# Performance work log

Measured on AMD Instinct MI355X. Metric: run time of the kernel, lower is better.

## Reference

```python
import jax, jax.numpy as jnp
from jax import lax
import numpy as np

N, CIN, COUT, H, W = 8, 64, 64, 256, 256
KH = KW = 3
AUX, HID = 128, 256


def setup_inputs() -> dict:
    key = jax.random.key(0)
    ks = jax.random.split(key, 12)
    k = float(np.sqrt(1.0 / (CIN * KH * KW)))
    inp = {
        "x": jax.random.normal(ks[0], (N, CIN, H, W), jnp.float32),
        "y": jax.random.normal(ks[1], (N, AUX), jnp.float32),
        "weight": jax.random.uniform(ks[2], (COUT, CIN, KH, KW), jnp.float32, -k, k),
        # modulation MLP: Linear(AUX->HID), PReLU, Linear(HID->COUT*CIN), Sigmoid
        "fc_w1": jax.random.normal(ks[3], (HID, AUX), jnp.float32) * 0.05,
        "fc_b1": jax.random.normal(ks[4], (HID,), jnp.float32) * 0.05,
        "fc_prelu": jnp.asarray(0.25, jnp.float32),
        "fc_w2": jax.random.normal(ks[5], (COUT * CIN, HID), jnp.float32) * 0.05,
        "fc_b2": jax.random.normal(ks[6], (COUT * CIN,), jnp.float32) * 0.05,
        # learned-bias MLP: Linear(AUX->HID), PReLU, Linear(HID->COUT)
        "bias_w1": jax.random.normal(ks[7], (HID, AUX), jnp.float32) * 0.05,
        "bias_b1": jax.random.normal(ks[8], (HID,), jnp.float32) * 0.05,
        "bias_prelu": jnp.asarray(0.25, jnp.float32),
        "bias_w2": jax.random.normal(ks[9], (COUT, HID), jnp.float32) * 0.05,
        "bias_b2": jax.random.normal(ks[10], (COUT,), jnp.float32) * 0.05,
    }
    return inp


def _prelu(h, a):
    return jnp.where(h >= 0, h, a * h)


def reference(x, y, weight, fc_w1, fc_b1, fc_prelu, fc_w2, fc_b2,
              bias_w1, bias_b1, bias_prelu, bias_w2, bias_b2):
    n, cin, h_, w_ = x.shape
    cout = weight.shape[0]
    # modulation factors: (N, COUT*CIN), sigmoid activation
    hm = _prelu(y @ fc_w1.T + fc_b1, fc_prelu)
    mod = jax.nn.sigmoid(hm @ fc_w2.T + fc_b2)
    # per-sample modulated kernels: (N, COUT, CIN, KH, KW)
    w_mod = mod.reshape(n, cout, cin, 1, 1) * weight
    # grouped conv with groups = batch, expressed as vmap over batch
    def conv1(xi, wi):  # xi: (CIN,H,W), wi: (COUT,CIN,KH,KW)
        return lax.conv_general_dilated(
            xi[None], wi, window_strides=(1, 1), padding=[(1, 1), (1, 1)],
            rhs_dilation=(1, 1))[0]
    out = jax.vmap(conv1)(x, w_mod)  # (N, COUT, H, W)
    # learned per-sample bias
    hb = _prelu(y @ bias_w1.T + bias_b1, bias_prelu)
    b = hb @ bias_w2.T + bias_b2  # (N, COUT)
    return out + b[:, :, None, None]
```

## Files before the change

kernel.cpp:

```cpp
#include <hip/hip_runtime.h>
#include <hip/hip_bf16.h>


typedef short bf16x8 __attribute__((ext_vector_type(8)));
typedef float f32x16 __attribute__((ext_vector_type(16)));

#define NB 8
#define CIN 64
#define COUT 64
#define HH 256
#define WW 256
#define HWP (HH * WW)
#define AUXD 128
#define HIDD 256

#define XRW8 (258 * 16)
#define XBUF8 (6 * XRW8)
#define WOFF (2 * XBUF8)
#define WUNITS (9 * 8 * 64)
#define SMEMB (WOFF + (WUNITS + 1) * 16)

__device__ __forceinline__ unsigned short f2bf(float f) {
    unsigned u = __builtin_bit_cast(unsigned, f);
    u += 0x7FFFu + ((u >> 16) & 1u);
    return (unsigned short)(u >> 16);
}

__device__ __forceinline__ unsigned pk2(float a, float b, float vm) {
    return (unsigned)f2bf(a * vm) | ((unsigned)f2bf(b * vm) << 16);
}

__global__ __launch_bounds__(256) void mlp_kernel(
    const float* __restrict__ y, const float* __restrict__ weight,
    const float* __restrict__ fc_w1, const float* __restrict__ fc_b1,
    const float* __restrict__ fc_prelu,
    const float* __restrict__ fc_w2, const float* __restrict__ fc_b2,
    const float* __restrict__ bias_w1, const float* __restrict__ bias_b1,
    const float* __restrict__ bias_prelu,
    const float* __restrict__ bias_w2, const float* __restrict__ bias_b2,
    unsigned short* __restrict__ w_bf, float* __restrict__ bvec)
{
    const int n = blockIdx.y;
    const int c = blockIdx.x;
    const int tid = threadIdx.x;
    __shared__ float ylds[AUXD];
    __shared__ float hl[HIDD];
    if (tid < AUXD) ylds[tid] = y[n * AUXD + tid];
    __syncthreads();

    if (c < 16) {
        float s = fc_b1[tid];
        const float* wrow = fc_w1 + tid * AUXD;
        #pragma unroll 4
        for (int a = 0; a < AUXD; ++a) s += ylds[a] * wrow[a];
        float ap = fc_prelu[0];
        hl[tid] = s >= 0.f ? s : ap * s;
        __syncthreads();

        int o = c * 256 + tid;
        float t = fc_b2[o];
        const float* w2row = fc_w2 + o * HIDD;
        #pragma unroll 4
        for (int h = 0; h < HIDD; ++h) t += hl[h] * w2row[h];
        float mod = 1.f / (1.f + expf(-t));
        int cout = o >> 6, ci = o & 63;
        int cb = ci >> 3, cl = ci & 7;
        #pragma unroll
        for (int k = 0; k < 9; ++k) {
            float wv = weight[o * 9 + k];
            w_bf[((((n * 9 + k) * 8 + cb) * 64 + cout) << 3) + cl] = f2bf(mod * wv);
        }
    } else {
        float s = bias_b1[tid];
        const float* wrow = bias_w1 + tid * AUXD;
        #pragma unroll 4
        for (int a = 0; a < AUXD; ++a) s += ylds[a] * wrow[a];
        float ap = bias_prelu[0];
        hl[tid] = s >= 0.f ? s : ap * s;
        __syncthreads();
        if (tid < COUT) {
            float t = bias_b2[tid];
            const float* w2row = bias_w2 + tid * HIDD;
            #pragma unroll 4
            for (int h = 0; h < HIDD; ++h) t += hl[h] * w2row[h];
            bvec[n * COUT + tid] = t;
        }
    }
}

#define XISSUE(stv, xp, ci0) { _Pragma("unroll") \
    for (int i = 0; i < 8; ++i) stv[i] = (xp)[(size_t)((ci0) + i) * HWP]; }

#define XWRITE(stv, rr, vmv, buf) { uint4 v_; \
    v_.x = pk2(stv[0], stv[1], vmv); v_.y = pk2(stv[2], stv[3], vmv); \
    v_.z = pk2(stv[4], stv[5], vmv); v_.w = pk2(stv[6], stv[7], vmv); \
    *(uint4*)((buf) + (rr) * XRW8 + (w + 1) * 16) = v_; }

__global__ __launch_bounds__(1024, 4) void conv_kernel(
    const float* __restrict__ x, const unsigned short* __restrict__ w_bf,
    const float* __restrict__ bvec, float* __restrict__ out)
{
    __shared__ __align__(16) unsigned char smem[SMEMB];

    const int bid = blockIdx.x;
    const int n = bid & 7;
    const int h0 = (bid >> 3) * 4;

    const int tid = threadIdx.x;
    const int lane = tid & 63;
    const int wave = tid >> 6;
    const int wr = wave >> 2;
    const int wq = wave & 3;
    const int l5 = lane >> 5;
    const int l31 = lane & 31;

    const int w = tid & 255;
    const int r0 = tid >> 8;
    const bool has2 = (tid < 512);
    const int r1 = 4 + (tid >> 8);

    int hin0 = h0 - 1 + r0;
    bool v0 = (hin0 >= 0) && (hin0 < HH);
    const float vm0 = v0 ? 1.f : 0.f;
    const float* xp0 = x + (size_t)n * CIN * HWP + (size_t)(v0 ? hin0 : 0) * WW + w;
    int hin1 = h0 - 1 + r1;
    bool v1 = (hin1 >= 0) && (hin1 < HH);
    const float vm1 = v1 ? 1.f : 0.f;
    const float* xp1 = x + (size_t)n * CIN * HWP + (size_t)(v1 ? hin1 : 0) * WW + w;

    {
        const uint4* wsrc = (const uint4*)w_bf + (size_t)n * WUNITS;
        #pragma unroll
        for (int it = 0; it < 5; ++it) {
            int u = it * 1024 + tid;
            if (u < WUNITS) *(uint4*)(smem + WOFF + (u << 4)) = wsrc[u];
        }
    }
    if (tid < 24) {
        int buf = tid / 12, rr = (tid % 12) >> 1, side = tid & 1;
        uint4 z; z.x = z.y = z.z = z.w = 0u;
        *(uint4*)(smem + buf * XBUF8 + rr * XRW8 + (side ? 257 : 0) * 16) = z;
    }
    if (tid == 24) {
        uint4 z; z.x = z.y = z.z = z.w = 0u;
        *(uint4*)(smem + WOFF + (WUNITS << 4)) = z;
    }

    float stA[8], stB[8];
    XISSUE(stA, xp0, 0);
    XWRITE(stA, r0, vm0, smem);
    if (has2) { XISSUE(stB, xp1, 0); XWRITE(stB, r1, vm1, smem); }

    f32x16 acc[2][2];
    #pragma unroll
    for (int m = 0; m < 2; ++m) {
        #pragma unroll
        for (int reg = 0; reg < 16; ++reg)
            acc[m][0][reg] = bvec[n * COUT + m * 32 + (reg & 3) + 8 * (reg >> 2) + 4 * l5];
        acc[m][1] = acc[m][0];
    }

    asm volatile("s_waitcnt lgkmcnt(0)" ::: "memory");
    __builtin_amdgcn_s_barrier();

    for (int c = 0; c < 8; ++c) {
        const int p = c & 1;
        const unsigned char* rbuf = smem + p * XBUF8;
        unsigned char* nx = smem + (p ^ 1) * XBUF8;
        const bool more = (c < 7);
        const int nci = (c + 1) * 8;

        #pragma unroll
        for (int s = 0; s < 5; ++s) {
            const int ka = 2 * s;
            const int kb = (s == 4) ? 8 : 2 * s + 1;
            const bool solo = (s == 4);
            const int khA = ka / 3, kwA = ka % 3;
            const int khB = kb / 3, kwB = kb % 3;
            const int kh = l5 ? khB : khA;
            const int kw = l5 ? kwB : kwA;

            int au = (solo && l5) ? WUNITS : ((l5 ? kb : ka) * 8 + c) * 64 + l31;
            int am = (solo && l5) ? 0 : 32;
            bf16x8 aA = *(const bf16x8*)(smem + WOFF + (au << 4));
            bf16x8 aB = *(const bf16x8*)(smem + WOFF + ((au + am) << 4));

            const unsigned char* bb = rbuf + (wr + kh) * XRW8;
            bf16x8 b0 = *(const bf16x8*)(bb + ((wq * 64 + l31 + kw) << 4));
            bf16x8 b1 = *(const bf16x8*)(bb + ((wq * 64 + 32 + l31 + kw) << 4));

            if (more) {
                if (s == 0)              { XISSUE(stA, xp0, nci); }
                else if (s == 1 && has2) { XISSUE(stB, xp1, nci); }
                else if (s == 3)         { XWRITE(stA, r0, vm0, nx); }
                else if (s == 4 && has2) { XWRITE(stB, r1, vm1, nx); }
            }

            __builtin_amdgcn_s_setprio(1);
            acc[0][0] = __builtin_amdgcn_mfma_f32_32x32x16_bf16(aA, b0, acc[0][0], 0, 0, 0);
            acc[0][1] = __builtin_amdgcn_mfma_f32_32x32x16_bf16(aA, b1, acc[0][1], 0, 0, 0);
            acc[1][0] = __builtin_amdgcn_mfma_f32_32x32x16_bf16(aB, b0, acc[1][0], 0, 0, 0);
            acc[1][1] = __builtin_amdgcn_mfma_f32_32x32x16_bf16(aB, b1, acc[1][1], 0, 0, 0);
            __builtin_amdgcn_s_setprio(0);
        }

        asm volatile("s_waitcnt lgkmcnt(0)" ::: "memory");
        __builtin_amdgcn_s_barrier();
    }

    const int hout = h0 + wr;
    float* ob = out + ((size_t)n * COUT * HH + hout) * WW;
    #pragma unroll
    for (int m = 0; m < 2; ++m) {
        #pragma unroll
        for (int j = 0; j < 2; ++j) {
            int colb = wq * 64 + j * 32 + l31;
            #pragma unroll
            for (int reg = 0; reg < 16; ++reg) {
                int cout = m * 32 + (reg & 3) + 8 * (reg >> 2) + 4 * l5;
                ob[(size_t)cout * HWP + colb] = acc[m][j][reg];
            }
        }
    }
}

extern "C" void kernel_launch(void* const* d_in, const int* in_sizes, int n_in,
                              void* d_out, int out_size, void* d_ws, size_t ws_size,
                              hipStream_t stream) {
    const float* x          = (const float*)d_in[0];
    const float* y          = (const float*)d_in[1];
    const float* weight     = (const float*)d_in[2];
    const float* fc_w1      = (const float*)d_in[3];
    const float* fc_b1      = (const float*)d_in[4];
    const float* fc_prelu   = (const float*)d_in[5];
    const float* fc_w2      = (const float*)d_in[6];
    const float* fc_b2      = (const float*)d_in[7];
    const float* bias_w1    = (const float*)d_in[8];
    const float* bias_b1    = (const float*)d_in[9];
    const float* bias_prelu = (const float*)d_in[10];
    const float* bias_w2    = (const float*)d_in[11];
    const float* bias_b2    = (const float*)d_in[12];
    float* out = (float*)d_out;

    unsigned short* w_bf = (unsigned short*)d_ws;
    float* bvec = (float*)((char*)d_ws + (size_t)NB * 9 * 64 * 64 * 2);

    hipLaunchKernelGGL(mlp_kernel, dim3(17, 8), dim3(256), 0, stream,
                       y, weight, fc_w1, fc_b1, fc_prelu, fc_w2, fc_b2,
                       bias_w1, bias_b1, bias_prelu, bias_w2, bias_b2, w_bf, bvec);
    hipLaunchKernelGGL(conv_kernel, dim3(512), dim3(1024), 0, stream,
                       x, w_bf, bvec, out);
}
```

Baseline: 87.37 us.

## Halve conv block to 2 output rows and prefetch input two chunks ahead

The conv kernel now uses 512-thread blocks that each compute 2 output rows instead of 4, doubling the grid to 1024 blocks and shrinking the input halo buffer from 6 to 4 rows. Input loads are issued two channel chunks ahead through a double-buffered register stage, with the chunk loop fully unrolled, to hide global load latency behind MFMA work. The trade-off is that the halo fraction rises from 1.5x to 2x rows, and each block still loads the full 72 KB per-sample weight set, so weight traffic into LDS doubles across the grid. Register pressure also grows from the extra staging.

Result: slower. 91.78 us (+5.1%).

```diff
diff --git a/kernel.cpp b/kernel.cpp
--- a/kernel.cpp
+++ b/kernel.cpp
@@ -15,7 +15,7 @@
 #define HIDD 256
 
 #define XRW8 (258 * 16)
-#define XBUF8 (6 * XRW8)
+#define XBUF8 (4 * XRW8)
 #define WOFF (2 * XBUF8)
 #define WUNITS (9 * 8 * 64)
 #define SMEMB (WOFF + (WUNITS + 1) * 16)
@@ -88,15 +88,21 @@
     }
 }
 
-#define XISSUE(stv, xp, ci0) { _Pragma("unroll") \
-    for (int i = 0; i < 8; ++i) stv[i] = (xp)[(size_t)((ci0) + i) * HWP]; }
-
-#define XWRITE(stv, rr, vmv, buf) { uint4 v_; \
-    v_.x = pk2(stv[0], stv[1], vmv); v_.y = pk2(stv[2], stv[3], vmv); \
-    v_.z = pk2(stv[4], stv[5], vmv); v_.w = pk2(stv[6], stv[7], vmv); \
-    *(uint4*)((buf) + (rr) * XRW8 + (w + 1) * 16) = v_; }
-
-__global__ __launch_bounds__(1024, 4) void conv_kernel(
+#define XISSUE0(g, cc) { _Pragma("unroll") \
+    for (int i = 0; i < 8; ++i) stg[g][0][i] = xp0[(size_t)((cc) * 8 + i) * HWP]; }
+#define XISSUE1(g, cc) { _Pragma("unroll") \
+    for (int i = 0; i < 8; ++i) stg[g][1][i] = xp1[(size_t)((cc) * 8 + i) * HWP]; }
+
+#define XWRITE0(g, buf) { uint4 v_; const float* s_ = stg[g][0]; \
+    v_.x = pk2(s_[0], s_[1], vm0); v_.y = pk2(s_[2], s_[3], vm0); \
+    v_.z = pk2(s_[4], s_[5], vm0); v_.w = pk2(s_[6], s_[7], vm0); \
+    *(uint4*)((buf) + r0 * XRW8 + (w + 1) * 16) = v_; }
+#define XWRITE1(g, buf) { uint4 v_; const float* s_ = stg[g][1]; \
+    v_.x = pk2(s_[0], s_[1], vm1); v_.y = pk2(s_[2], s_[3], vm1); \
+    v_.z = pk2(s_[4], s_[5], vm1); v_.w = pk2(s_[6], s_[7], vm1); \
+    *(uint4*)((buf) + r1 * XRW8 + (w + 1) * 16) = v_; }
+
+__global__ __launch_bounds__(512, 2) void conv_kernel(
     const float* __restrict__ x, const unsigned short* __restrict__ w_bf,
     const float* __restrict__ bvec, float* __restrict__ out)
 {
@@ -104,7 +110,7 @@
 
     const int bid = blockIdx.x;
     const int n = bid & 7;
-    const int h0 = (bid >> 3) * 4;
+    const int h0 = (bid >> 3) * 2;
 
     const int tid = threadIdx.x;
     const int lane = tid & 63;
@@ -116,8 +122,7 @@
 
     const int w = tid & 255;
     const int r0 = tid >> 8;
-    const bool has2 = (tid < 512);
-    const int r1 = 4 + (tid >> 8);
+    const int r1 = r0 + 2;
 
     int hin0 = h0 - 1 + r0;
     bool v0 = (hin0 >= 0) && (hin0 < HH);
@@ -131,25 +136,26 @@
     {
         const uint4* wsrc = (const uint4*)w_bf + (size_t)n * WUNITS;
         #pragma unroll
-        for (int it = 0; it < 5; ++it) {
-            int u = it * 1024 + tid;
-            if (u < WUNITS) *(uint4*)(smem + WOFF + (u << 4)) = wsrc[u];
-        }
-    }
-    if (tid < 24) {
-        int buf = tid / 12, rr = (tid % 12) >> 1, side = tid & 1;
+        for (int it = 0; it < 9; ++it) {
+            int u = it * 512 + tid;
+            *(uint4*)(smem + WOFF + (u << 4)) = wsrc[u];
+        }
+    }
+    if (tid < 16) {
+        int buf = tid >> 3, rr = (tid >> 1) & 3, side = tid & 1;
         uint4 z; z.x = z.y = z.z = z.w = 0u;
         *(uint4*)(smem + buf * XBUF8 + rr * XRW8 + (side ? 257 : 0) * 16) = z;
     }
-    if (tid == 24) {
+    if (tid == 16) {
         uint4 z; z.x = z.y = z.z = z.w = 0u;
         *(uint4*)(smem + WOFF + (WUNITS << 4)) = z;
     }
 
-    float stA[8], stB[8];
-    XISSUE(stA, xp0, 0);
-    XWRITE(stA, r0, vm0, smem);
-    if (has2) { XISSUE(stB, xp1, 0); XWRITE(stB, r1, vm1, smem); }
+    float stg[2][2][8];
+
+    XISSUE0(0, 0); XISSUE1(0, 0);
+    XWRITE0(0, smem); XWRITE1(0, smem);
+    XISSUE0(1, 1); XISSUE1(1, 1);
 
     f32x16 acc[2][2];
     #pragma unroll
@@ -163,12 +169,11 @@
     asm volatile("s_waitcnt lgkmcnt(0)" ::: "memory");
     __builtin_amdgcn_s_barrier();
 
+    #pragma unroll
     for (int c = 0; c < 8; ++c) {
         const int p = c & 1;
         const unsigned char* rbuf = smem + p * XBUF8;
         unsigned char* nx = smem + (p ^ 1) * XBUF8;
-        const bool more = (c < 7);
-        const int nci = (c + 1) * 8;
 
         #pragma unroll
         for (int s = 0; s < 5; ++s) {
@@ -189,12 +194,10 @@
             bf16x8 b0 = *(const bf16x8*)(bb + ((wq * 64 + l31 + kw) << 4));
             bf16x8 b1 = *(const bf16x8*)(bb + ((wq * 64 + 32 + l31 + kw) << 4));
 
-            if (more) {
-                if (s == 0)              { XISSUE(stA, xp0, nci); }
-                else if (s == 1 && has2) { XISSUE(stB, xp1, nci); }
-                else if (s == 3)         { XWRITE(stA, r0, vm0, nx); }
-                else if (s == 4 && has2) { XWRITE(stB, r1, vm1, nx); }
-            }
+            if (s == 0 && c < 6) { XISSUE0(p, c + 2); }
+            if (s == 1 && c < 6) { XISSUE1(p, c + 2); }
+            if (s == 3 && c < 7) { XWRITE0(p ^ 1, nx); }
+            if (s == 4 && c < 7) { XWRITE1(p ^ 1, nx); }
 
             __builtin_amdgcn_s_setprio(1);
             acc[0][0] = __builtin_amdgcn_mfma_f32_32x32x16_bf16(aA, b0, acc[0][0], 0, 0, 0);
@@ -248,6 +251,6 @@
     hipLaunchKernelGGL(mlp_kernel, dim3(17, 8), dim3(256), 0, stream,
                        y, weight, fc_w1, fc_b1, fc_prelu, fc_w2, fc_b2,
                        bias_w1, bias_b1, bias_prelu, bias_w2, bias_b2, w_bf, bvec);
-    hipLaunchKernelGGL(conv_kernel, dim3(512), dim3(1024), 0, stream,
+    hipLaunchKernelGGL(conv_kernel, dim3(1024), dim3(512), 0, stream,
                        x, w_bf, bvec, out);
 }
```
